# Performance work log

Measured on AMD Instinct MI355X. Metric: run time of the kernel, lower is better.

Reference implementation:

```python
import jax, jax.numpy as jnp
import numpy as np
import math

D = 512      # d_model = sd_dim*2
DFF = 512    # dim_feedforward
S = 512      # num_seg (queries)
T = 32768    # video frames (keys)
RATE = 4     # self-attention band half-width
SCALE = 1.0 / math.sqrt(D)


def _ln(x, g, b):
    m = x.mean(-1, keepdims=True)
    v = ((x - m) ** 2).mean(-1, keepdims=True)
    return (x - m) / jnp.sqrt(v + 1e-5) * g + b


def setup_inputs() -> dict:
    key = jax.random.key(0)
    ks = jax.random.split(key, 12)
    w = lambda k, shp, s=0.02: jax.random.normal(k, shp, jnp.float32) * s
    # exactly S contiguous action segments over T frames
    action_idx = jnp.asarray((np.arange(T) * S) // T, dtype=jnp.int32)
    return dict(
        tgt=w(ks[0], (S, 1, D), 1.0), memory=w(ks[1], (T, 1, D), 1.0),
        pos=w(ks[2], (T, 1, D), 0.1), query_pos=w(ks[3], (S, 1, D), 0.1),
        action_idx=action_idx,
        ca_t2l_w=w(ks[4], (D, D)), ca_t2l_b=jnp.zeros(D),
        ca_l1_w=w(ks[5], (DFF, D)), ca_l1_b=jnp.zeros(DFF),
        ca_l2_w=w(ks[6], (D, DFF)), ca_l2_b=jnp.zeros(D),
        ca_n2_g=jnp.ones(D), ca_n2_b=jnp.zeros(D),
        ca_n3_g=jnp.ones(D), ca_n3_b=jnp.zeros(D),
        sa_conv_w=w(ks[7], (D, D)), sa_conv_b=jnp.zeros(D),
        sa_l1_w=w(ks[8], (DFF, D)), sa_l1_b=jnp.zeros(DFF),
        sa_l2_w=w(ks[9], (D, DFF)), sa_l2_b=jnp.zeros(D),
        sa_n1_g=jnp.ones(D), sa_n1_b=jnp.zeros(D),
        sa_n2_g=jnp.ones(D), sa_n2_b=jnp.zeros(D),
    )


def reference(tgt, memory, pos, query_pos, action_idx,
              ca_t2l_w, ca_t2l_b, ca_l1_w, ca_l1_b, ca_l2_w, ca_l2_b,
              ca_n2_g, ca_n2_b, ca_n3_g, ca_n3_b,
              sa_conv_w, sa_conv_b, sa_l1_w, sa_l1_b, sa_l2_w, sa_l2_b,
              sa_n1_g, sa_n1_b, sa_n2_g, sa_n2_b):
    # ---------------- CrossAttention (segment mask) ----------------
    q = tgt + query_pos                      # (S,1,D)
    k = memory + pos                         # (T,1,D)
    scores = jnp.einsum('sbd,tbd->bst', q, k) * SCALE   # (1,S,T)
    # segment id per frame from change points of action_idx
    chg = (action_idx[1:] != action_idx[:-1]).astype(jnp.int32)
    seg_id = jnp.concatenate([jnp.zeros(1, jnp.int32), jnp.cumsum(chg)])  # (T,)
    # query i attends to segments i-1, i, i+1
    mask = jnp.abs(seg_id[None, :] - jnp.arange(S, dtype=jnp.int32)[:, None]) <= 1  # (S,T)
    scores = jnp.where(mask[None], scores, -jnp.inf)
    attn = jax.nn.softmax(scores, axis=-1)               # (1,S,T)
    tgt2 = jnp.einsum('bst,tbd->sbd', attn, memory)      # (S,1,D)
    tgt2 = jnp.maximum(tgt2, 0.0) @ ca_t2l_w.T + ca_t2l_b
    x = _ln(tgt + tgt2, ca_n2_g, ca_n2_b)
    ffn = jnp.maximum(x @ ca_l1_w.T + ca_l1_b, 0.0) @ ca_l2_w.T + ca_l2_b
    x = _ln(x + ffn, ca_n3_g, ca_n3_b)                   # (S,1,D)
    # ---------------- SelfAttention (banded, pos=None) ----------------
    src = jnp.transpose(x, (1, 0, 2))                    # (1,S,D)
    s2 = jnp.einsum('bsd,btd->bst', src, src) * SCALE    # (1,S,S)
    i = jnp.arange(S)
    band = jnp.abs(i[:, None] - i[None, :]) <= RATE      # (S,S)
    s2 = jnp.where(band[None], s2, -jnp.inf)
    a2 = jax.nn.softmax(s2, axis=-1)                     # (1,S,S)
    src2 = jnp.einsum('bqk,bkd->bqd', a2, src)           # (1,S,D)
    src2 = jnp.maximum(src2, 0.0) @ sa_conv_w.T + sa_conv_b  # 1x1 conv over channels
    y = _ln(src + src2, sa_n1_g, sa_n1_b)
    ffn2 = jnp.maximum(y @ sa_l1_w.T + sa_l1_b, 0.0) @ sa_l2_w.T + sa_l2_b
    y = _ln(y + ffn2, sa_n2_g, sa_n2_b)
    return y                                              # (1,S,D)
```

## Files before the change

kernel.cpp:

```cpp
#include <hip/hip_runtime.h>

#define S_Q 512
#define DIM 512
#define SCALE_F 0.04419417382415922f
#define LDS_W 520

typedef short short8 __attribute__((ext_vector_type(8)));
typedef float floatx4 __attribute__((ext_vector_type(4)));

__device__ __forceinline__ float wave_sum(float v) {
#pragma unroll
  for (int o = 32; o > 0; o >>= 1) v += __shfl_xor(v, o);
  return v;
}
__device__ __forceinline__ unsigned short f2bf(float f) {
  unsigned u = __float_as_uint(f);
  return (unsigned short)((u + 0x7FFFu + ((u >> 16) & 1u)) >> 16);
}
__device__ __forceinline__ float bf2f(short s) {
  return __uint_as_float(((unsigned)(unsigned short)s) << 16);
}

__device__ __forceinline__ void gload16(const void* g, void* l) {
  __builtin_amdgcn_global_load_lds(
      (const __attribute__((address_space(1))) unsigned int*)g,
      (__attribute__((address_space(3))) unsigned int*)l, 16, 0, 0);
}

__global__ __launch_bounds__(256) void k_ca_partial(
    const float* __restrict__ tgt, const float* __restrict__ qpos,
    const float* __restrict__ mem, const float* __restrict__ pos,
    unsigned short* __restrict__ part_acc, float* __restrict__ part_ms) {
  const int j = blockIdx.x;
  const int tid = threadIdx.x;
  const int w = tid >> 6, lane = tid & 63;
  __shared__ short q_hi[4][LDS_W];
  __shared__ short q_lo[4][LDS_W];
  __shared__ float stage_mem[4][2][16 * 32];
  __shared__ float stage_pos[4][2][16 * 32];
  __shared__ float p_lds[4][3][16];
  __shared__ float wacc[4][3][DIM];
  __shared__ float wms[4][3][2];

  {
    const int d0 = lane * 8;
    const int qi = j - 1 + w;
    if (w < 3 && (unsigned)qi < (unsigned)S_Q) {
      float4 t0 = *(const float4*)(tgt + (size_t)qi * DIM + d0);
      float4 t1 = *(const float4*)(tgt + (size_t)qi * DIM + d0 + 4);
      float4 q0 = *(const float4*)(qpos + (size_t)qi * DIM + d0);
      float4 q1 = *(const float4*)(qpos + (size_t)qi * DIM + d0 + 4);
      float v[8] = {t0.x + q0.x, t0.y + q0.y, t0.z + q0.z, t0.w + q0.w,
                    t1.x + q1.x, t1.y + q1.y, t1.z + q1.z, t1.w + q1.w};
      short8 hi, lo;
#pragma unroll
      for (int e = 0; e < 8; ++e) {
        unsigned short h = f2bf(v[e]);
        hi[e] = (short)h;
        lo[e] = (short)f2bf(v[e] - bf2f((short)h));
      }
      *(short8*)(&q_hi[w][d0]) = hi;
      *(short8*)(&q_lo[w][d0]) = lo;
    } else {
      short8 z = {0, 0, 0, 0, 0, 0, 0, 0};
      *(short8*)(&q_hi[w][d0]) = z;
      *(short8*)(&q_lo[w][d0]) = z;
    }
  }
  __syncthreads();

  const int arow = lane & 15;
  const int kgrp = lane >> 4;
  const int qrow = (arow < 3) ? arow : 3;
  const float* mrow = mem + ((size_t)j * 64 + w * 16) * DIM;
  const float* prow = pos + ((size_t)j * 64 + w * 16) * DIM;
  const int sfrm = lane >> 3;
  const int sorg = (((lane & 7) ^ (lane >> 3)) << 4);

#define CA_ISSUE(KC, BUF)                                                    \
  do {                                                                       \
    const char* gm = (const char*)(mrow + (size_t)sfrm * DIM) + (KC)*128 + sorg; \
    const char* gp = (const char*)(prow + (size_t)sfrm * DIM) + (KC)*128 + sorg; \
    gload16(gm, (void*)&stage_mem[w][BUF][0]);                               \
    gload16(gm + 8 * DIM * 4, (void*)&stage_mem[w][BUF][256]);               \
    gload16(gp, (void*)&stage_pos[w][BUF][0]);                               \
    gload16(gp + 8 * DIM * 4, (void*)&stage_pos[w][BUF][256]);               \
  } while (0)

  CA_ISSUE(0, 0);

  floatx4 acc_hh = {0.f, 0.f, 0.f, 0.f};
  floatx4 acc_lh = {0.f, 0.f, 0.f, 0.f};
  floatx4 acc_hl = {0.f, 0.f, 0.f, 0.f};
  const int sw = (arow & 7) << 4;
  const int rowb = arow * 128;
  const int cA = rowb + (((kgrp * 32) + 0) ^ sw);
  const int cB = rowb + (((kgrp * 32) + 16) ^ sw);

  for (int kc = 0; kc < 16; ++kc) {
    const int cur = kc & 1;
    if (kc < 15) {
      CA_ISSUE(kc + 1, cur ^ 1);
      asm volatile("s_waitcnt vmcnt(4)" ::: "memory");
    } else {
      asm volatile("s_waitcnt vmcnt(0)" ::: "memory");
    }
    const char* smb = (const char*)&stage_mem[w][cur][0];
    const char* spb = (const char*)&stage_pos[w][cur][0];
    const float4 mA = *(const float4*)(smb + cA);
    const float4 mB = *(const float4*)(smb + cB);
    const float4 pA = *(const float4*)(spb + cA);
    const float4 pB = *(const float4*)(spb + cB);
    float kv[8] = {mA.x + pA.x, mA.y + pA.y, mA.z + pA.z, mA.w + pA.w,
                   mB.x + pB.x, mB.y + pB.y, mB.z + pB.z, mB.w + pB.w};
    short8 ah, al;
#pragma unroll
    for (int e = 0; e < 8; ++e) {
      unsigned short h = f2bf(kv[e]);
      ah[e] = (short)h;
      al[e] = (short)f2bf(kv[e] - bf2f((short)h));
    }
    const int qcol = kc * 32 + kgrp * 8;
    const short8 qh = *(const short8*)(&q_hi[qrow][qcol]);
    const short8 ql = *(const short8*)(&q_lo[qrow][qcol]);
    acc_hh = __builtin_amdgcn_mfma_f32_16x16x32_bf16(ah, qh, acc_hh, 0, 0, 0);
    acc_lh = __builtin_amdgcn_mfma_f32_16x16x32_bf16(al, qh, acc_lh, 0, 0, 0);
    acc_hl = __builtin_amdgcn_mfma_f32_16x16x32_bf16(ah, ql, acc_hl, 0, 0, 0);
  }
#undef CA_ISSUE

  float s[4];
#pragma unroll
  for (int r = 0; r < 4; ++r)
    s[r] = (acc_hh[r] + acc_lh[r] + acc_hl[r]) * SCALE_F;
  float mloc = fmaxf(fmaxf(s[0], s[1]), fmaxf(s[2], s[3]));
  mloc = fmaxf(mloc, __shfl_xor(mloc, 16));
  mloc = fmaxf(mloc, __shfl_xor(mloc, 32));
  float p[4], sloc = 0.f;
#pragma unroll
  for (int r = 0; r < 4; ++r) {
    p[r] = __expf(s[r] - mloc);
    sloc += p[r];
  }
  sloc += __shfl_xor(sloc, 16);
  sloc += __shfl_xor(sloc, 32);
  if (arow < 3) {
    *(float4*)(&p_lds[w][arow][kgrp * 4]) = make_float4(p[0], p[1], p[2], p[3]);
    if (lane < 3) {
      wms[w][lane][0] = mloc;
      wms[w][lane][1] = sloc;
    }
  }

  const int d0 = lane * 8;
  float acc[3][8];
#pragma unroll
  for (int c = 0; c < 3; ++c)
#pragma unroll
    for (int e = 0; e < 8; ++e) acc[c][e] = 0.f;
  const float* mb = mem + ((size_t)j * 64 + w * 16) * DIM + d0;
#pragma unroll 4
  for (int f = 0; f < 16; ++f) {
    float4 m0 = *(const float4*)(mb + (size_t)f * DIM);
    float4 m1 = *(const float4*)(mb + (size_t)f * DIM + 4);
    const float mv[8] = {m0.x, m0.y, m0.z, m0.w, m1.x, m1.y, m1.z, m1.w};
    const float w0 = p_lds[w][0][f];
    const float w1 = p_lds[w][1][f];
    const float w2 = p_lds[w][2][f];
#pragma unroll
    for (int e = 0; e < 8; ++e) {
      acc[0][e] += w0 * mv[e];
      acc[1][e] += w1 * mv[e];
      acc[2][e] += w2 * mv[e];
    }
  }

#pragma unroll
  for (int c = 0; c < 3; ++c) {
    *(float4*)(&wacc[w][c][d0]) =
        make_float4(acc[c][0], acc[c][1], acc[c][2], acc[c][3]);
    *(float4*)(&wacc[w][c][d0 + 4]) =
        make_float4(acc[c][4], acc[c][5], acc[c][6], acc[c][7]);
  }
  __syncthreads();

  const int d = tid * 2;
#pragma unroll
  for (int c = 0; c < 3; ++c) {
    const int qi = j - 1 + c;
    if ((unsigned)qi >= (unsigned)S_Q) continue;
    float M = wms[0][c][0];
#pragma unroll
    for (int u = 1; u < 4; ++u) M = fmaxf(M, wms[u][c][0]);
    float S = 0.f, ax = 0.f, ay = 0.f;
#pragma unroll
    for (int u = 0; u < 4; ++u) {
      const float wg = __expf(wms[u][c][0] - M);
      S += wg * wms[u][c][1];
      const float2 a = *(const float2*)(&wacc[u][c][d]);
      ax += wg * a.x;
      ay += wg * a.y;
    }
    const size_t slot = (size_t)qi * 3 + c;
    unsigned* dst = (unsigned*)(part_acc + slot * DIM + d);
    *dst = (unsigned)f2bf(ax) | ((unsigned)f2bf(ay) << 16);
    if (tid == 0) {
      part_ms[slot * 2 + 0] = M;
      part_ms[slot * 2 + 1] = S;
    }
  }
}

__device__ __forceinline__ void stage_tile(const float* __restrict__ G,
                                           short* __restrict__ Ls,
                                           int rowblk, int tid) {
  const int w = tid >> 6, lane = tid & 63;
  const int col = lane * 8;
#pragma unroll
  for (int u = 0; u < 8; ++u) {
    const int row = u * 4 + w;
    const float* src = G + (size_t)(rowblk * 32 + row) * DIM + col;
    float4 a = *(const float4*)src;
    float4 b = *(const float4*)(src + 4);
    short8 s;
    s[0] = (short)f2bf(a.x); s[1] = (short)f2bf(a.y);
    s[2] = (short)f2bf(a.z); s[3] = (short)f2bf(a.w);
    s[4] = (short)f2bf(b.x); s[5] = (short)f2bf(b.y);
    s[6] = (short)f2bf(b.z); s[7] = (short)f2bf(b.w);
    *(short8*)(&Ls[row * LDS_W + col]) = s;
  }
}

template <bool RELU>
__device__ __forceinline__ void gemm_core(const short* __restrict__ As,
                                          const short* __restrict__ Ws,
                                          const float* __restrict__ bias,
                                          float* __restrict__ C, int bx, int by,
                                          int wave, int lane) {
  const int r0 = (wave >> 1) * 16, c0 = (wave & 1) * 16;
  const int frow = lane & 15, fk = (lane >> 4) * 8;
  const short* ap = &As[(r0 + frow) * LDS_W + fk];
  const short* wp = &Ws[(c0 + frow) * LDS_W + fk];
  floatx4 acc = {0.f, 0.f, 0.f, 0.f};
#pragma unroll
  for (int kc = 0; kc < 16; ++kc) {
    const short8 af = *(const short8*)(ap + kc * 32);
    const short8 wf = *(const short8*)(wp + kc * 32);
    acc = __builtin_amdgcn_mfma_f32_16x16x32_bf16(af, wf, acc, 0, 0, 0);
  }
  const int col = bx * 32 + c0 + frow;
  const int rowb = by * 32 + r0 + (lane >> 4) * 4;
  const float b = bias[col];
#pragma unroll
  for (int r = 0; r < 4; ++r) {
    float v = acc[r] + b;
    if (RELU) v = fmaxf(v, 0.f);
    C[(size_t)(rowb + r) * DIM + col] = v;
  }
}

__device__ __forceinline__ void ln_prologue(const float* __restrict__ X,
                                            const float* __restrict__ R,
                                            const float* __restrict__ g,
                                            const float* __restrict__ b,
                                            short* __restrict__ As, int by,
                                            float* x_out, int wave, int lane) {
  const int d0 = lane * 8;
  float gg[8], bb[8];
  {
    float4 g0 = *(const float4*)(g + d0);
    float4 g1 = *(const float4*)(g + d0 + 4);
    float4 b0 = *(const float4*)(b + d0);
    float4 b1 = *(const float4*)(b + d0 + 4);
    gg[0] = g0.x; gg[1] = g0.y; gg[2] = g0.z; gg[3] = g0.w;
    gg[4] = g1.x; gg[5] = g1.y; gg[6] = g1.z; gg[7] = g1.w;
    bb[0] = b0.x; bb[1] = b0.y; bb[2] = b0.z; bb[3] = b0.w;
    bb[4] = b1.x; bb[5] = b1.y; bb[6] = b1.z; bb[7] = b1.w;
  }
  for (int r = wave; r < 32; r += 4) {
    const int grow = by * 32 + r;
    const float* xp = X + (size_t)grow * DIM + d0;
    const float* rp = R + (size_t)grow * DIM + d0;
    float4 x0 = *(const float4*)xp;
    float4 x1 = *(const float4*)(xp + 4);
    float4 r0 = *(const float4*)rp;
    float4 r1 = *(const float4*)(rp + 4);
    float v[8] = {x0.x + r0.x, x0.y + r0.y, x0.z + r0.z, x0.w + r0.w,
                  x1.x + r1.x, x1.y + r1.y, x1.z + r1.z, x1.w + r1.w};
    float s = 0.f, sq = 0.f;
#pragma unroll
    for (int e = 0; e < 8; ++e) { s += v[e]; sq += v[e] * v[e]; }
#pragma unroll
    for (int o = 32; o > 0; o >>= 1) {
      s += __shfl_xor(s, o);
      sq += __shfl_xor(sq, o);
    }
    const float mean = s * (1.f / DIM);
    const float var = sq * (1.f / DIM) - mean * mean;
    const float rstd = rsqrtf(var + 1e-5f);
    float o8[8];
    short8 sv;
#pragma unroll
    for (int e = 0; e < 8; ++e) {
      o8[e] = (v[e] - mean) * rstd * gg[e] + bb[e];
      sv[e] = (short)f2bf(o8[e]);
    }
    *(short8*)(&As[r * LDS_W + d0]) = sv;
    if (x_out) {
      *(float4*)(x_out + (size_t)grow * DIM + d0) =
          make_float4(o8[0], o8[1], o8[2], o8[3]);
      *(float4*)(x_out + (size_t)grow * DIM + d0 + 4) =
          make_float4(o8[4], o8[5], o8[6], o8[7]);
    }
  }
}

__global__ __launch_bounds__(256) void k_g1(
    const unsigned short* __restrict__ part_acc,
    const float* __restrict__ part_ms, const float* __restrict__ W,
    const float* __restrict__ bias, float* __restrict__ C) {
  __shared__ short As[32 * LDS_W];
  __shared__ short Ws[32 * LDS_W];
  const int tid = threadIdx.x;
  const int bx = blockIdx.x, by = blockIdx.y;
  const int wave = tid >> 6, lane = tid & 63;
  const int d0 = lane * 8;
  for (int r = wave; r < 32; r += 4) {
    const int i = by * 32 + r;
    const bool valid[3] = {i < S_Q - 1, true, i > 0};
    float mm[3], ss[3], M = -1e30f;
#pragma unroll
    for (int c = 0; c < 3; ++c) {
      if (valid[c]) {
        mm[c] = part_ms[((size_t)i * 3 + c) * 2 + 0];
        ss[c] = part_ms[((size_t)i * 3 + c) * 2 + 1];
        M = fmaxf(M, mm[c]);
      } else {
        mm[c] = -1e30f;
        ss[c] = 0.f;
      }
    }
    float den = 0.f, wg[3];
#pragma unroll
    for (int c = 0; c < 3; ++c) {
      wg[c] = valid[c] ? __expf(mm[c] - M) : 0.f;
      den += wg[c] * ss[c];
    }
    const float inv = 1.f / den;
    float o[8] = {0.f, 0.f, 0.f, 0.f, 0.f, 0.f, 0.f, 0.f};
#pragma unroll
    for (int c = 0; c < 3; ++c) {
      if (valid[c]) {
        const short8 pa =
            *(const short8*)(part_acc + ((size_t)i * 3 + c) * DIM + d0);
#pragma unroll
        for (int e = 0; e < 8; ++e) o[e] += wg[c] * bf2f(pa[e]);
      }
    }
    short8 sv;
#pragma unroll
    for (int e = 0; e < 8; ++e) sv[e] = (short)f2bf(fmaxf(o[e] * inv, 0.f));
    *(short8*)(&As[r * LDS_W + d0]) = sv;
  }
  stage_tile(W, Ws, bx, tid);
  __syncthreads();
  gemm_core<false>(As, Ws, bias, C, bx, by, wave, lane);
}

__global__ __launch_bounds__(256) void k_gln(
    const float* __restrict__ X, const float* __restrict__ R,
    const float* __restrict__ g, const float* __restrict__ b,
    const float* __restrict__ W, const float* __restrict__ bias,
    float* __restrict__ C, float* __restrict__ x_out) {
  __shared__ short As[32 * LDS_W];
  __shared__ short Ws[32 * LDS_W];
  const int tid = threadIdx.x;
  const int bx = blockIdx.x, by = blockIdx.y;
  const int wave = tid >> 6, lane = tid & 63;
  ln_prologue(X, R, g, b, As, by, (bx == 0) ? x_out : nullptr, wave, lane);
  stage_tile(W, Ws, bx, tid);
  __syncthreads();
  gemm_core<true>(As, Ws, bias, C, bx, by, wave, lane);
}

__global__ __launch_bounds__(256) void k_gplain(
    const float* __restrict__ A, const float* __restrict__ W,
    const float* __restrict__ bias, float* __restrict__ C) {
  __shared__ short As[32 * LDS_W];
  __shared__ short Ws[32 * LDS_W];
  const int tid = threadIdx.x;
  const int bx = blockIdx.x, by = blockIdx.y;
  const int wave = tid >> 6, lane = tid & 63;
  stage_tile(A, As, by, tid);
  stage_tile(W, Ws, bx, tid);
  __syncthreads();
  gemm_core<false>(As, Ws, bias, C, bx, by, wave, lane);
}

__global__ __launch_bounds__(256) void k_g4(
    const float* __restrict__ X, const float* __restrict__ R,
    const float* __restrict__ g, const float* __restrict__ b,
    const float* __restrict__ W, const float* __restrict__ bias,
    float* __restrict__ C, float* __restrict__ x2_out) {
  __shared__ short Xw[40 * LDS_W];
  __shared__ short As[32 * LDS_W];
  __shared__ short Ws[32 * LDS_W];
  const int tid = threadIdx.x;
  const int bx = blockIdx.x, by = blockIdx.y;
  const int wave = tid >> 6, lane = tid & 63;
  const int d0 = lane * 8;
  const int wlo = (by * 32 - 4 > 0) ? by * 32 - 4 : 0;
  const int whi = (by * 32 + 35 < S_Q - 1) ? by * 32 + 35 : S_Q - 1;
  const int nw = whi - wlo + 1;

  {
    float gg[8], bb[8];
    float4 g0 = *(const float4*)(g + d0);
    float4 g1 = *(const float4*)(g + d0 + 4);
    float4 b0 = *(const float4*)(b + d0);
    float4 b1 = *(const float4*)(b + d0 + 4);
    gg[0] = g0.x; gg[1] = g0.y; gg[2] = g0.z; gg[3] = g0.w;
    gg[4] = g1.x; gg[5] = g1.y; gg[6] = g1.z; gg[7] = g1.w;
    bb[0] = b0.x; bb[1] = b0.y; bb[2] = b0.z; bb[3] = b0.w;
    bb[4] = b1.x; bb[5] = b1.y; bb[6] = b1.z; bb[7] = b1.w;
    for (int r = wave; r < nw; r += 4) {
      const int grow = wlo + r;
      const float* xp = X + (size_t)grow * DIM + d0;
      const float* rp = R + (size_t)grow * DIM + d0;
      float4 x0 = *(const float4*)xp;
      float4 x1 = *(const float4*)(xp + 4);
      float4 r0 = *(const float4*)rp;
      float4 r1 = *(const float4*)(rp + 4);
      float v[8] = {x0.x + r0.x, x0.y + r0.y, x0.z + r0.z, x0.w + r0.w,
                    x1.x + r1.x, x1.y + r1.y, x1.z + r1.z, x1.w + r1.w};
      float s = 0.f, sq = 0.f;
#pragma unroll
      for (int e = 0; e < 8; ++e) { s += v[e]; sq += v[e] * v[e]; }
#pragma unroll
      for (int o = 32; o > 0; o >>= 1) {
        s += __shfl_xor(s, o);
        sq += __shfl_xor(sq, o);
      }
      const float mean = s * (1.f / DIM);
      const float var = sq * (1.f / DIM) - mean * mean;
      const float rstd = rsqrtf(var + 1e-5f);
      float o8[8];
      short8 sv;
#pragma unroll
      for (int e = 0; e < 8; ++e) {
        o8[e] = (v[e] - mean) * rstd * gg[e] + bb[e];
        sv[e] = (short)f2bf(o8[e]);
      }
      *(short8*)(&Xw[r * LDS_W + d0]) = sv;
      if (bx == 0 && grow >= by * 32 && grow < by * 32 + 32) {
        *(float4*)(x2_out + (size_t)grow * DIM + d0) =
            make_float4(o8[0], o8[1], o8[2], o8[3]);
        *(float4*)(x2_out + (size_t)grow * DIM + d0 + 4) =
            make_float4(o8[4], o8[5], o8[6], o8[7]);
      }
    }
  }
  stage_tile(W, Ws, bx, tid);
  __syncthreads();

  for (int li = wave; li < 32; li += 4) {
    const int i = by * 32 + li;
    const int lq = i - wlo;
    float qv[8];
    {
      const short8 qs = *(const short8*)(&Xw[lq * LDS_W + d0]);
#pragma unroll
      for (int e = 0; e < 8; ++e) qv[e] = bf2f(qs[e]);
    }
    const int jlo = (i - 4 > 0) ? i - 4 : 0;
    const int jhi = (i + 4 < S_Q - 1) ? i + 4 : S_Q - 1;
    const int n = jhi - jlo + 1;
    float sc[9];
#pragma unroll
    for (int k = 0; k < 9; ++k) {
      if (k < n) {
        const int lk = jlo + k - wlo;
        const short8 ks = *(const short8*)(&Xw[lk * LDS_W + d0]);
        float dd = 0.f;
#pragma unroll
        for (int e = 0; e < 8; ++e) dd += qv[e] * bf2f(ks[e]);
        sc[k] = dd;
      } else {
        sc[k] = 0.f;
      }
    }
#pragma unroll
    for (int o = 32; o > 0; o >>= 1)
#pragma unroll
      for (int k = 0; k < 9; ++k) sc[k] += __shfl_xor(sc[k], o);
    float M = -1e30f;
#pragma unroll
    for (int k = 0; k < 9; ++k) {
      sc[k] *= SCALE_F;
      if (k < n) M = fmaxf(M, sc[k]);
    }
    float p[9], den = 0.f;
#pragma unroll
    for (int k = 0; k < 9; ++k) {
      p[k] = (k < n) ? __expf(sc[k] - M) : 0.f;
      den += p[k];
    }
    const float inv = 1.f / den;
    float o8[8] = {0.f, 0.f, 0.f, 0.f, 0.f, 0.f, 0.f, 0.f};
#pragma unroll
    for (int k = 0; k < 9; ++k) {
      if (k < n) {
        const int lk = jlo + k - wlo;
        const short8 ks = *(const short8*)(&Xw[lk * LDS_W + d0]);
#pragma unroll
        for (int e = 0; e < 8; ++e) o8[e] += p[k] * bf2f(ks[e]);
      }
    }
    short8 sv;
#pragma unroll
    for (int e = 0; e < 8; ++e) sv[e] = (short)f2bf(fmaxf(o8[e] * inv, 0.f));
    *(short8*)(&As[li * LDS_W + d0]) = sv;
  }
  __syncthreads();
  gemm_core<false>(As, Ws, bias, C, bx, by, wave, lane);
}

__global__ __launch_bounds__(256) void k_addln(
    const float* __restrict__ X, const float* __restrict__ R,
    const float* __restrict__ g, const float* __restrict__ b,
    float* __restrict__ out) {
  const int row = blockIdx.x * 4 + (threadIdx.x >> 6);
  const int lane = threadIdx.x & 63;
  const int d = lane * 8;
  const float4* xp = (const float4*)(X + (size_t)row * DIM + d);
  const float4* rp = (const float4*)(R + (size_t)row * DIM + d);
  float4 x0 = xp[0], x1 = xp[1], r0 = rp[0], r1 = rp[1];
  float v[8] = {x0.x + r0.x, x0.y + r0.y, x0.z + r0.z, x0.w + r0.w,
                x1.x + r1.x, x1.y + r1.y, x1.z + r1.z, x1.w + r1.w};
  float s = 0.f, sq = 0.f;
#pragma unroll
  for (int e = 0; e < 8; ++e) { s += v[e]; sq += v[e] * v[e]; }
  s = wave_sum(s);
  sq = wave_sum(sq);
  const float mean = s * (1.f / DIM);
  const float var = sq * (1.f / DIM) - mean * mean;
  const float rstd = rsqrtf(var + 1e-5f);
  const float4* gp = (const float4*)(g + d);
  const float4* bp = (const float4*)(b + d);
  float4 g0 = gp[0], g1 = gp[1], bb0 = bp[0], bb1 = bp[1];
  float4 o0, o1;
  o0.x = (v[0] - mean) * rstd * g0.x + bb0.x;
  o0.y = (v[1] - mean) * rstd * g0.y + bb0.y;
  o0.z = (v[2] - mean) * rstd * g0.z + bb0.z;
  o0.w = (v[3] - mean) * rstd * g0.w + bb0.w;
  o1.x = (v[4] - mean) * rstd * g1.x + bb1.x;
  o1.y = (v[5] - mean) * rstd * g1.y + bb1.y;
  o1.z = (v[6] - mean) * rstd * g1.z + bb1.z;
  o1.w = (v[7] - mean) * rstd * g1.w + bb1.w;
  *(float4*)(out + (size_t)row * DIM + d) = o0;
  *(float4*)(out + (size_t)row * DIM + d + 4) = o1;
}

extern "C" void kernel_launch(void* const* d_in, const int* in_sizes, int n_in,
                              void* d_out, int out_size, void* d_ws, size_t ws_size,
                              hipStream_t stream) {
  const float* tgt       = (const float*)d_in[0];
  const float* memory    = (const float*)d_in[1];
  const float* pos       = (const float*)d_in[2];
  const float* qpos      = (const float*)d_in[3];
  const float* ca_t2l_w  = (const float*)d_in[5];
  const float* ca_t2l_b  = (const float*)d_in[6];
  const float* ca_l1_w   = (const float*)d_in[7];
  const float* ca_l1_b   = (const float*)d_in[8];
  const float* ca_l2_w   = (const float*)d_in[9];
  const float* ca_l2_b   = (const float*)d_in[10];
  const float* ca_n2_g   = (const float*)d_in[11];
  const float* ca_n2_b   = (const float*)d_in[12];
  const float* ca_n3_g   = (const float*)d_in[13];
  const float* ca_n3_b   = (const float*)d_in[14];
  const float* sa_conv_w = (const float*)d_in[15];
  const float* sa_conv_b = (const float*)d_in[16];
  const float* sa_l1_w   = (const float*)d_in[17];
  const float* sa_l1_b   = (const float*)d_in[18];
  const float* sa_l2_w   = (const float*)d_in[19];
  const float* sa_l2_b   = (const float*)d_in[20];
  const float* sa_n1_g   = (const float*)d_in[21];
  const float* sa_n1_b   = (const float*)d_in[22];
  const float* sa_n2_g   = (const float*)d_in[23];
  const float* sa_n2_b   = (const float*)d_in[24];
  float* out = (float*)d_out;
  float* ws = (float*)d_ws;

  unsigned short* part_acc = (unsigned short*)ws;
  float* part_ms = ws + 393216;
  float* t2 = ws + 396288;
  float* h  = ws + 658432;
  float* x  = ws + 920576;
  float* f  = ws + 0;
  float* x2 = ws + 396288;
  float* c  = ws + 658432;
  float* y1 = ws + 0;
  float* h2 = ws + 920576;
  float* f2 = ws + 396288;

  const dim3 gg(16, 16, 1);

  k_ca_partial<<<512, 256, 0, stream>>>(tgt, qpos, memory, pos, part_acc, part_ms);
  k_g1<<<gg, 256, 0, stream>>>(part_acc, part_ms, ca_t2l_w, ca_t2l_b, t2);
  k_gln<<<gg, 256, 0, stream>>>(tgt, t2, ca_n2_g, ca_n2_b, ca_l1_w, ca_l1_b, h, x);
  k_gplain<<<gg, 256, 0, stream>>>(h, ca_l2_w, ca_l2_b, f);
  k_g4<<<gg, 256, 0, stream>>>(x, f, ca_n3_g, ca_n3_b, sa_conv_w, sa_conv_b, c, x2);
  k_gln<<<gg, 256, 0, stream>>>(x2, c, sa_n1_g, sa_n1_b, sa_l1_w, sa_l1_b, h2, y1);
  k_gplain<<<gg, 256, 0, stream>>>(h2, sa_l2_w, sa_l2_b, f2);
  k_addln<<<128, 256, 0, stream>>>(f2, y1, sa_n2_g, sa_n2_b, out);
}
```

Baseline: 287.9 us.

## Fuse GEMM chains into per-row-block kernels with redundant recompute

After: 366.1 us. +27.2%, slower.

```diff
diff --git a/kernel.cpp b/kernel.cpp
--- a/kernel.cpp
+++ b/kernel.cpp
@@ -4,6 +4,7 @@
 #define DIM 512
 #define SCALE_F 0.04419417382415922f
 #define LDS_W 520
+#define CF_W 516
 
 typedef short short8 __attribute__((ext_vector_type(8)));
 typedef float floatx4 __attribute__((ext_vector_type(4)));
@@ -231,6 +232,18 @@
   }
 }
 
+__device__ __forceinline__ floatx4 gemm_tile_acc(const short* __restrict__ ap,
+                                                 const short* __restrict__ wp) {
+  floatx4 acc = {0.f, 0.f, 0.f, 0.f};
+#pragma unroll
+  for (int kc = 0; kc < 16; ++kc) {
+    const short8 af = *(const short8*)(ap + kc * 32);
+    const short8 wf = *(const short8*)(wp + kc * 32);
+    acc = __builtin_amdgcn_mfma_f32_16x16x32_bf16(af, wf, acc, 0, 0, 0);
+  }
+  return acc;
+}
+
 template <bool RELU>
 __device__ __forceinline__ void gemm_core(const short* __restrict__ As,
                                           const short* __restrict__ Ws,
@@ -239,15 +252,8 @@
                                           int wave, int lane) {
   const int r0 = (wave >> 1) * 16, c0 = (wave & 1) * 16;
   const int frow = lane & 15, fk = (lane >> 4) * 8;
-  const short* ap = &As[(r0 + frow) * LDS_W + fk];
-  const short* wp = &Ws[(c0 + frow) * LDS_W + fk];
-  floatx4 acc = {0.f, 0.f, 0.f, 0.f};
-#pragma unroll
-  for (int kc = 0; kc < 16; ++kc) {
-    const short8 af = *(const short8*)(ap + kc * 32);
-    const short8 wf = *(const short8*)(wp + kc * 32);
-    acc = __builtin_amdgcn_mfma_f32_16x16x32_bf16(af, wf, acc, 0, 0, 0);
-  }
+  floatx4 acc =
+      gemm_tile_acc(&As[(r0 + frow) * LDS_W + fk], &Ws[(c0 + frow) * LDS_W + fk]);
   const int col = bx * 32 + c0 + frow;
   const int rowb = by * 32 + r0 + (lane >> 4) * 4;
   const float b = bias[col];
@@ -257,6 +263,37 @@
     if (RELU) v = fmaxf(v, 0.f);
     C[(size_t)(rowb + r) * DIM + col] = v;
   }
+}
+
+__device__ __forceinline__ void gemm_tile_to_f32lds(
+    const short* __restrict__ As, const short* __restrict__ Ws,
+    const float* __restrict__ bias, float* __restrict__ Cf, int wt, int wave,
+    int lane) {
+  const int r0 = (wave >> 1) * 16, c0 = (wave & 1) * 16;
+  const int frow = lane & 15, fk = (lane >> 4) * 8;
+  floatx4 acc =
+      gemm_tile_acc(&As[(r0 + frow) * LDS_W + fk], &Ws[(c0 + frow) * LDS_W + fk]);
+  const int col = wt * 32 + c0 + frow;
+  const int rowb = r0 + (lane >> 4) * 4;
+  const float b = bias[col];
+#pragma unroll
+  for (int r = 0; r < 4; ++r) Cf[(rowb + r) * CF_W + col] = acc[r] + b;
+}
+
+__device__ __forceinline__ void gemm_tile_to_bf16lds_relu(
+    const short* __restrict__ As, const short* __restrict__ Ws,
+    const float* __restrict__ bias, short* __restrict__ Hb, int wt, int wave,
+    int lane) {
+  const int r0 = (wave >> 1) * 16, c0 = (wave & 1) * 16;
+  const int frow = lane & 15, fk = (lane >> 4) * 8;
+  floatx4 acc =
+      gemm_tile_acc(&As[(r0 + frow) * LDS_W + fk], &Ws[(c0 + frow) * LDS_W + fk]);
+  const int col = wt * 32 + c0 + frow;
+  const int rowb = r0 + (lane >> 4) * 4;
+  const float b = bias[col];
+#pragma unroll
+  for (int r = 0; r < 4; ++r)
+    Hb[(rowb + r) * LDS_W + col] = (short)f2bf(fmaxf(acc[r] + b, 0.f));
 }
 
 __device__ __forceinline__ void ln_prologue(const float* __restrict__ X,
@@ -315,16 +352,23 @@
   }
 }
 
-__global__ __launch_bounds__(256) void k_g1(
+__global__ __launch_bounds__(256) void k_t1(
     const unsigned short* __restrict__ part_acc,
-    const float* __restrict__ part_ms, const float* __restrict__ W,
-    const float* __restrict__ bias, float* __restrict__ C) {
+    const float* __restrict__ part_ms, const float* __restrict__ tgt,
+    const float* __restrict__ Wt2l, const float* __restrict__ bt2l,
+    const float* __restrict__ W1, const float* __restrict__ b1,
+    const float* __restrict__ W2, const float* __restrict__ b2,
+    const float* __restrict__ n2g, const float* __restrict__ n2b,
+    float* __restrict__ x_out, float* __restrict__ f_out) {
   __shared__ short As[32 * LDS_W];
   __shared__ short Ws[32 * LDS_W];
+  __shared__ float T2f[32 * CF_W];
+  short* Hb = (short*)T2f;
   const int tid = threadIdx.x;
   const int bx = blockIdx.x, by = blockIdx.y;
   const int wave = tid >> 6, lane = tid & 63;
   const int d0 = lane * 8;
+
   for (int r = wave; r < 32; r += 4) {
     const int i = by * 32 + r;
     const bool valid[3] = {i < S_Q - 1, true, i > 0};
@@ -362,39 +406,73 @@
     for (int e = 0; e < 8; ++e) sv[e] = (short)f2bf(fmaxf(o[e] * inv, 0.f));
     *(short8*)(&As[r * LDS_W + d0]) = sv;
   }
-  stage_tile(W, Ws, bx, tid);
-  __syncthreads();
-  gemm_core<false>(As, Ws, bias, C, bx, by, wave, lane);
-}
-
-__global__ __launch_bounds__(256) void k_gln(
-    const float* __restrict__ X, const float* __restrict__ R,
-    const float* __restrict__ g, const float* __restrict__ b,
-    const float* __restrict__ W, const float* __restrict__ bias,
-    float* __restrict__ C, float* __restrict__ x_out) {
-  __shared__ short As[32 * LDS_W];
-  __shared__ short Ws[32 * LDS_W];
-  const int tid = threadIdx.x;
-  const int bx = blockIdx.x, by = blockIdx.y;
-  const int wave = tid >> 6, lane = tid & 63;
-  ln_prologue(X, R, g, b, As, by, (bx == 0) ? x_out : nullptr, wave, lane);
-  stage_tile(W, Ws, bx, tid);
-  __syncthreads();
-  gemm_core<true>(As, Ws, bias, C, bx, by, wave, lane);
-}
-
-__global__ __launch_bounds__(256) void k_gplain(
-    const float* __restrict__ A, const float* __restrict__ W,
-    const float* __restrict__ bias, float* __restrict__ C) {
-  __shared__ short As[32 * LDS_W];
-  __shared__ short Ws[32 * LDS_W];
-  const int tid = threadIdx.x;
-  const int bx = blockIdx.x, by = blockIdx.y;
-  const int wave = tid >> 6, lane = tid & 63;
-  stage_tile(A, As, by, tid);
-  stage_tile(W, Ws, bx, tid);
-  __syncthreads();
-  gemm_core<false>(As, Ws, bias, C, bx, by, wave, lane);
+
+  for (int wt = 0; wt < 16; ++wt) {
+    __syncthreads();
+    stage_tile(Wt2l, Ws, wt, tid);
+    __syncthreads();
+    gemm_tile_to_f32lds(As, Ws, bt2l, T2f, wt, wave, lane);
+  }
+  __syncthreads();
+
+  {
+    float gg[8], bb[8];
+    float4 g0 = *(const float4*)(n2g + d0);
+    float4 g1 = *(const float4*)(n2g + d0 + 4);
+    float4 b0 = *(const float4*)(n2b + d0);
+    float4 b1 = *(const float4*)(n2b + d0 + 4);
+    gg[0] = g0.x; gg[1] = g0.y; gg[2] = g0.z; gg[3] = g0.w;
+    gg[4] = g1.x; gg[5] = g1.y; gg[6] = g1.z; gg[7] = g1.w;
+    bb[0] = b0.x; bb[1] = b0.y; bb[2] = b0.z; bb[3] = b0.w;
+    bb[4] = b1.x; bb[5] = b1.y; bb[6] = b1.z; bb[7] = b1.w;
+    for (int r = wave; r < 32; r += 4) {
+      const int grow = by * 32 + r;
+      const float* tp = tgt + (size_t)grow * DIM + d0;
+      float4 t0 = *(const float4*)tp;
+      float4 t1 = *(const float4*)(tp + 4);
+      const float* trow = &T2f[r * CF_W + d0];
+      float v[8] = {t0.x + trow[0], t0.y + trow[1], t0.z + trow[2],
+                    t0.w + trow[3], t1.x + trow[4], t1.y + trow[5],
+                    t1.z + trow[6], t1.w + trow[7]};
+      float s = 0.f, sq = 0.f;
+#pragma unroll
+      for (int e = 0; e < 8; ++e) { s += v[e]; sq += v[e] * v[e]; }
+#pragma unroll
+      for (int o = 32; o > 0; o >>= 1) {
+        s += __shfl_xor(s, o);
+        sq += __shfl_xor(sq, o);
+      }
+      const float mean = s * (1.f / DIM);
+      const float var = sq * (1.f / DIM) - mean * mean;
+      const float rstd = rsqrtf(var + 1e-5f);
+      float o8[8];
+      short8 sv;
+#pragma unroll
+      for (int e = 0; e < 8; ++e) {
+        o8[e] = (v[e] - mean) * rstd * gg[e] + bb[e];
+        sv[e] = (short)f2bf(o8[e]);
+      }
+      *(short8*)(&As[r * LDS_W + d0]) = sv;
+      if (bx == 0) {
+        *(float4*)(x_out + (size_t)grow * DIM + d0) =
+            make_float4(o8[0], o8[1], o8[2], o8[3]);
+        *(float4*)(x_out + (size_t)grow * DIM + d0 + 4) =
+            make_float4(o8[4], o8[5], o8[6], o8[7]);
+      }
+    }
+  }
+
+  for (int wt = 0; wt < 16; ++wt) {
+    __syncthreads();
+    stage_tile(W1, Ws, wt, tid);
+    __syncthreads();
+    gemm_tile_to_bf16lds_relu(As, Ws, b1, Hb, wt, wave, lane);
+  }
+
+  __syncthreads();
+  stage_tile(W2, Ws, bx, tid);
+  __syncthreads();
+  gemm_core<false>(Hb, Ws, b2, f_out, bx, by, wave, lane);
 }
 
 __global__ __launch_bounds__(256) void k_g4(
@@ -523,6 +601,34 @@
   }
   __syncthreads();
   gemm_core<false>(As, Ws, bias, C, bx, by, wave, lane);
+}
+
+__global__ __launch_bounds__(256) void k_t2(
+    const float* __restrict__ x2, const float* __restrict__ c,
+    const float* __restrict__ n1g, const float* __restrict__ n1b,
+    const float* __restrict__ Wl1, const float* __restrict__ bl1,
+    const float* __restrict__ Wl2, const float* __restrict__ bl2,
+    float* __restrict__ y1_out, float* __restrict__ f2_out) {
+  __shared__ short As[32 * LDS_W];
+  __shared__ short Ws[32 * LDS_W];
+  __shared__ short Hb2[32 * LDS_W];
+  const int tid = threadIdx.x;
+  const int bx = blockIdx.x, by = blockIdx.y;
+  const int wave = tid >> 6, lane = tid & 63;
+
+  ln_prologue(x2, c, n1g, n1b, As, by, (bx == 0) ? y1_out : nullptr, wave, lane);
+
+  for (int wt = 0; wt < 16; ++wt) {
+    __syncthreads();
+    stage_tile(Wl1, Ws, wt, tid);
+    __syncthreads();
+    gemm_tile_to_bf16lds_relu(As, Ws, bl1, Hb2, wt, wave, lane);
+  }
+
+  __syncthreads();
+  stage_tile(Wl2, Ws, bx, tid);
+  __syncthreads();
+  gemm_core<false>(Hb2, Ws, bl2, f2_out, bx, by, wave, lane);
 }
 
 __global__ __launch_bounds__(256) void k_addln(
@@ -593,24 +699,21 @@
 
   unsigned short* part_acc = (unsigned short*)ws;
   float* part_ms = ws + 393216;
-  float* t2 = ws + 396288;
-  float* h  = ws + 658432;
-  float* x  = ws + 920576;
-  float* f  = ws + 0;
-  float* x2 = ws + 396288;
-  float* c  = ws + 658432;
-  float* y1 = ws + 0;
-  float* h2 = ws + 920576;
-  float* f2 = ws + 396288;
+  float* x  = ws + 396288;
+  float* f  = ws + 658432;
+  float* c  = ws + 0;
+  float* x2 = ws + 920576;
+  float* y1 = ws + 396288;
+  float* f2 = ws + 658432;
 
   const dim3 gg(16, 16, 1);
 
   k_ca_partial<<<512, 256, 0, stream>>>(tgt, qpos, memory, pos, part_acc, part_ms);
-  k_g1<<<gg, 256, 0, stream>>>(part_acc, part_ms, ca_t2l_w, ca_t2l_b, t2);
-  k_gln<<<gg, 256, 0, stream>>>(tgt, t2, ca_n2_g, ca_n2_b, ca_l1_w, ca_l1_b, h, x);
-  k_gplain<<<gg, 256, 0, stream>>>(h, ca_l2_w, ca_l2_b, f);
+  k_t1<<<gg, 256, 0, stream>>>(part_acc, part_ms, tgt, ca_t2l_w, ca_t2l_b,
+                               ca_l1_w, ca_l1_b, ca_l2_w, ca_l2_b, ca_n2_g,
+                               ca_n2_b, x, f);
   k_g4<<<gg, 256, 0, stream>>>(x, f, ca_n3_g, ca_n3_b, sa_conv_w, sa_conv_b, c, x2);
-  k_gln<<<gg, 256, 0, stream>>>(x2, c, sa_n1_g, sa_n1_b, sa_l1_w, sa_l1_b, h2, y1);
-  k_gplain<<<gg, 256, 0, stream>>>(h2, sa_l2_w, sa_l2_b, f2);
+  k_t2<<<gg, 256, 0, stream>>>(x2, c, sa_n1_g, sa_n1_b, sa_l1_w, sa_l1_b,
+                               sa_l2_w, sa_l2_b, y1, f2);
   k_addln<<<128, 256, 0, stream>>>(f2, y1, sa_n2_g, sa_n2_b, out);
 }
```
